# Performance work log

Measured on AMD Instinct MI355X. Metric: run time of the kernel, lower is better.

Reference implementation:

```python
import jax, jax.numpy as jnp
import numpy as np


def _gcn_conv(x, W, b, src, dst, n_nodes):
    """PyG-style GCNConv: XW, symmetric deg^-1/2 normalization over edges
    (with self-loops already included in src/dst), scatter-add to targets, + bias."""
    xw = x @ W  # [N, F_out]
    ones = jnp.ones(src.shape[0], dtype=xw.dtype)
    deg = jax.ops.segment_sum(ones, dst, num_segments=n_nodes)  # in-degree incl. self-loops
    dinv = jnp.where(deg > 0, jax.lax.rsqrt(jnp.maximum(deg, 1.0)), 0.0)
    norm = dinv[src] * dinv[dst]                        # [E]
    msgs = xw[src] * norm[:, None]                      # [E, F_out] gather + scale
    out = jax.ops.segment_sum(msgs, dst, num_segments=n_nodes)  # scatter-add
    return out + b


def setup_inputs() -> dict:
    key = jax.random.key(0)
    k1, k2, k3, k4 = jax.random.split(key, 4)
    N, E = 100000, 1600000
    IN, HID, OUT = 128, 64, 64
    x = jax.random.normal(k1, (N, IN), dtype=jnp.float32)
    edge_index = jax.random.randint(k2, (2, E), 0, N, dtype=jnp.int64)
    W1 = jax.random.normal(k3, (IN, HID), dtype=jnp.float32) * (1.0 / np.sqrt(IN))
    b1 = jnp.zeros((HID,), dtype=jnp.float32)
    W2 = jax.random.normal(k4, (HID, OUT), dtype=jnp.float32) * (1.0 / np.sqrt(HID))
    b2 = jnp.zeros((OUT,), dtype=jnp.float32)
    return {"x": x, "edge_index": edge_index, "W1": W1, "b1": b1, "W2": W2, "b2": b2}


def reference(x, edge_index, W1, b1, W2, b2):
    n_nodes = x.shape[0]
    # add self-loops (PyG GCNConv default add_self_loops=True)
    loops = jnp.arange(n_nodes, dtype=edge_index.dtype)
    src = jnp.concatenate([edge_index[0], loops])
    dst = jnp.concatenate([edge_index[1], loops])
    h = _gcn_conv(x, W1, b1, src, dst, n_nodes)
    h = jax.nn.relu(h)
    z = _gcn_conv(h, W2, b2, src, dst, n_nodes)
    return z
```

## Files before the change

kernel.cpp:

```cpp
#include <hip/hip_runtime.h>

#define IN_F 128
#define HID_F 64
#define BKT_SHIFT 9
#define BKT_SIZE 512
#define CHUNK 4096

typedef unsigned short ushort_t;
typedef __attribute__((ext_vector_type(8))) short bf16x8;
typedef __attribute__((ext_vector_type(8))) unsigned short u16x8;
typedef __attribute__((ext_vector_type(4))) float f32x4;

__device__ inline ushort_t f2bf(float f) {
    unsigned u = __float_as_uint(f);
    u += 0x7FFFu + ((u >> 16) & 1u);
    return (ushort_t)(u >> 16);
}
__device__ inline float bf2f(ushort_t u) {
    return __uint_as_float((unsigned)u << 16);
}


__global__ __launch_bounds__(256) void k_hist_pack(const int* __restrict__ dst,
        int* __restrict__ ghist, int E, int nbE,
        const float* __restrict__ W1, const float* __restrict__ W2,
        ushort_t* __restrict__ Bp1, ushort_t* __restrict__ Bp2) {
    int tid = threadIdx.x;
    if ((int)blockIdx.x >= nbE) {
        int id = ((int)blockIdx.x - nbE) * 256 + tid;
        int iw = (id < 8192) ? id : id - 8192;
        int j = iw & 7, lane = (iw >> 3) & 63, t = (iw >> 9) & 3, s = iw >> 11;
        int k = s * 32 + ((lane >> 4) << 3) + j;
        int n = t * 16 + (lane & 15);
        if (id < 8192)        Bp1[iw] = f2bf(W1[k * 64 + n]);
        else if (id < 12288)  Bp2[iw] = f2bf(W2[k * 64 + n]);
        return;
    }
    __shared__ int hist[256];
    hist[tid] = 0;
    __syncthreads();
    int e0 = blockIdx.x * CHUNK, e1 = min(e0 + CHUNK, E);
    for (int e = e0 + tid; e < e1; e += 256)
        atomicAdd(&hist[dst[e] >> BKT_SHIFT], 1);
    __syncthreads();
    ghist[blockIdx.x * 256 + tid] = hist[tid];
}

__global__ __launch_bounds__(256) void k_colscan(int* __restrict__ ghist,
        int* __restrict__ gcount, int nb) {
    __shared__ int s[256];
    int t = threadIdx.x;
    int b = blockIdx.x;
    int j0 = 2 * t, j1 = 2 * t + 1;
    int v0 = (j0 < nb) ? ghist[j0 * 256 + b] : 0;
    int v1 = (j1 < nb) ? ghist[j1 * 256 + b] : 0;
    int p = v0 + v1;
    s[t] = p;
    __syncthreads();
    for (int off = 1; off < 256; off <<= 1) {
        int v = (t >= off) ? s[t - off] : 0;
        __syncthreads();
        s[t] += v;
        __syncthreads();
    }
    int excl = s[t] - p;
    if (j0 < nb) ghist[j0 * 256 + b] = excl;
    if (j1 < nb) ghist[j1 * 256 + b] = excl + v0;
    if (t == 255) gcount[b] = s[255];
}

__global__ __launch_bounds__(256) void k_scatter(const int* __restrict__ src,
        const int* __restrict__ dst, const int* __restrict__ ghist,
        const int* __restrict__ gcount, unsigned* __restrict__ gbin, int E) {
    __shared__ int cur[256];
    __shared__ int s[256];
    int tid = threadIdx.x;
    int gc = gcount[tid];
    s[tid] = gc;
    __syncthreads();
    for (int off = 1; off < 256; off <<= 1) {
        int v = (tid >= off) ? s[tid - off] : 0;
        __syncthreads();
        s[tid] += v;
        __syncthreads();
    }
    cur[tid] = ghist[blockIdx.x * 256 + tid] + (s[tid] - gc);
    __syncthreads();
    int e0 = blockIdx.x * CHUNK, e1 = min(e0 + CHUNK, E);
    for (int e = e0 + tid; e < e1; e += 256) {
        int d = dst[e];
        int b = d >> BKT_SHIFT;
        int p = atomicAdd(&cur[b], 1);
        gbin[p] = ((unsigned)(d & (BKT_SIZE - 1)) << 23) | (unsigned)src[e];
    }
}

__global__ __launch_bounds__(256) void k_fill2(const unsigned* __restrict__ gbin,
        const int* __restrict__ gcount, int* __restrict__ rowptr,
        float* __restrict__ dinv, int* __restrict__ col, int N, int E) {
    __shared__ int cnt[BKT_SIZE];
    __shared__ int pos[BKT_SIZE];
    __shared__ int s[256];
    int tid = threadIdx.x;
    int b = blockIdx.x;
    int gc = gcount[tid];
    s[tid] = gc;
    __syncthreads();
    for (int off = 1; off < 256; off <<= 1) {
        int v = (tid >= off) ? s[tid - off] : 0;
        __syncthreads();
        s[tid] += v;
        __syncthreads();
    }
    int e0 = (b > 0) ? s[b - 1] : 0;
    int e1 = s[b];
    if (b == 0 && tid == 0) rowptr[N] = E;
    __syncthreads();
    cnt[tid] = 0; cnt[tid + 256] = 0;
    __syncthreads();
    for (int e = e0 + tid; e < e1; e += 256)
        atomicAdd(&cnt[gbin[e] >> 23], 1);
    __syncthreads();
    int c0 = cnt[2 * tid], c1 = cnt[2 * tid + 1];
    int p2 = c0 + c1;
    s[tid] = p2;
    __syncthreads();
    for (int off = 1; off < 256; off <<= 1) {
        int v = (tid >= off) ? s[tid - off] : 0;
        __syncthreads();
        s[tid] += v;
        __syncthreads();
    }
    int excl = s[tid] - p2;
    pos[2 * tid] = excl;
    pos[2 * tid + 1] = excl + c0;
    __syncthreads();
    int n0 = b << BKT_SHIFT;
    #pragma unroll
    for (int i = tid; i < BKT_SIZE; i += 256) {
        int n = n0 + i;
        if (n < N) {
            rowptr[n] = e0 + pos[i];
            dinv[n] = rsqrtf((float)cnt[i] + 1.0f);
        }
    }
    __syncthreads();
    for (int e = e0 + tid; e < e1; e += 256) {
        unsigned v = gbin[e];
        int p = atomicAdd(&pos[v >> 23], 1);
        col[e0 + p] = (int)(v & 0x7FFFFFu);
    }
}

template<int K, typename AT>
__global__ __launch_bounds__(256) void k_gemm_mfma(const AT* __restrict__ A,
        const ushort_t* __restrict__ Bp, const float* __restrict__ dinv,
        ushort_t* __restrict__ out, int N) {
    int wave = threadIdx.x >> 6, lane = threadIdx.x & 63;
    int m = lane & 15, q = lane >> 4;
    int row0 = blockIdx.x * 64 + wave * 16;
    int arow = row0 + m;
    int arowc = (arow < N) ? arow : (N - 1);
    f32x4 acc[4] = {};
    #pragma unroll
    for (int s = 0; s < K / 32; ++s) {
        bf16x8 af;
        if constexpr (sizeof(AT) == 4) {
            const float* ap = (const float*)A + (size_t)arowc * K + s * 32 + q * 8;
            float4 x0 = *(const float4*)ap;
            float4 x1 = *(const float4*)(ap + 4);
            af[0] = (short)f2bf(x0.x); af[1] = (short)f2bf(x0.y);
            af[2] = (short)f2bf(x0.z); af[3] = (short)f2bf(x0.w);
            af[4] = (short)f2bf(x1.x); af[5] = (short)f2bf(x1.y);
            af[6] = (short)f2bf(x1.z); af[7] = (short)f2bf(x1.w);
        } else {
            af = *(const bf16x8*)((const ushort_t*)A + (size_t)arowc * K + s * 32 + q * 8);
        }
        #pragma unroll
        for (int t = 0; t < 4; ++t) {
            bf16x8 bf = *(const bf16x8*)(Bp + (size_t)((s * 4 + t) * 64 + lane) * 8);
            acc[t] = __builtin_amdgcn_mfma_f32_16x16x32_bf16(af, bf, acc[t], 0, 0, 0);
        }
    }
    int orow0 = row0 + q * 4;
    float4 d4 = *(const float4*)(dinv + orow0);
    #pragma unroll
    for (int r = 0; r < 4; ++r) {
        int row = orow0 + r;
        if (row < N) {
            float dn = (r == 0) ? d4.x : (r == 1) ? d4.y : (r == 2) ? d4.z : d4.w;
            #pragma unroll
            for (int t = 0; t < 4; ++t)
                out[(size_t)row * 64 + t * 16 + m] = f2bf(acc[t][r] * dn);
        }
    }
}

__global__ __launch_bounds__(256) void k_agg_gemm(const ushort_t* __restrict__ xws,
        const int* __restrict__ rowptr, const int* __restrict__ col,
        const float* __restrict__ dinv, const float* __restrict__ bias,
        const ushort_t* __restrict__ Bp2, ushort_t* __restrict__ out2, int N) {
    __shared__ ushort_t hl[32][72];
    int tid = threadIdx.x;
    int nl = tid >> 3;
    int i = tid & 7;
    int n0 = blockIdx.x * 32;
    int n = n0 + nl;
    u16x8 hz = {};
    if (n < N) {
        int beg = rowptr[n], end = rowptr[n + 1];
        float dn = dinv[n];
        const ushort_t* base = xws + i * 8;
        u16x8 sv = *(const u16x8*)(base + (size_t)n * 64);
        float a[8];
        #pragma unroll
        for (int k = 0; k < 8; ++k) a[k] = bf2f(sv[k]);
        int e = beg;
        for (; e + 8 <= end; e += 8) {
            int c[8];
            #pragma unroll
            for (int j = 0; j < 8; ++j) c[j] = col[e + j];
            u16x8 v[8];
            #pragma unroll
            for (int j = 0; j < 8; ++j) v[j] = *(const u16x8*)(base + (size_t)c[j] * 64);
            #pragma unroll
            for (int j = 0; j < 8; ++j)
                #pragma unroll
                for (int k = 0; k < 8; ++k) a[k] += bf2f(v[j][k]);
        }
        if (e + 4 <= end) {
            int c[4];
            #pragma unroll
            for (int j = 0; j < 4; ++j) c[j] = col[e + j];
            u16x8 v[4];
            #pragma unroll
            for (int j = 0; j < 4; ++j) v[j] = *(const u16x8*)(base + (size_t)c[j] * 64);
            #pragma unroll
            for (int j = 0; j < 4; ++j)
                #pragma unroll
                for (int k = 0; k < 8; ++k) a[k] += bf2f(v[j][k]);
            e += 4;
        }
        for (; e < end; ++e) {
            u16x8 v = *(const u16x8*)(base + (size_t)col[e] * 64);
            #pragma unroll
            for (int k = 0; k < 8; ++k) a[k] += bf2f(v[k]);
        }
        float4 b0 = *(const float4*)(bias + i * 8);
        float4 b1 = *(const float4*)(bias + i * 8 + 4);
        float r[8];
        r[0] = dn * a[0] + b0.x; r[1] = dn * a[1] + b0.y;
        r[2] = dn * a[2] + b0.z; r[3] = dn * a[3] + b0.w;
        r[4] = dn * a[4] + b1.x; r[5] = dn * a[5] + b1.y;
        r[6] = dn * a[6] + b1.z; r[7] = dn * a[7] + b1.w;
        #pragma unroll
        for (int k = 0; k < 8; ++k) hz[k] = f2bf(fmaxf(r[k], 0.f));
    }
    *(u16x8*)&hl[nl][i * 8] = hz;
    __syncthreads();
    int w = tid >> 6, lane = tid & 63;
    int m = lane & 15, q = lane >> 4;
    int mt = w & 1;
    int nt0 = (w >> 1) << 1;
    f32x4 acc[2] = {};
    #pragma unroll
    for (int s = 0; s < 2; ++s) {
        bf16x8 af = *(const bf16x8*)&hl[mt * 16 + m][s * 32 + q * 8];
        #pragma unroll
        for (int tt = 0; tt < 2; ++tt) {
            bf16x8 bf = *(const bf16x8*)(Bp2 + (size_t)((s * 4 + nt0 + tt) * 64 + lane) * 8);
            acc[tt] = __builtin_amdgcn_mfma_f32_16x16x32_bf16(af, bf, acc[tt], 0, 0, 0);
        }
    }
    int orow0 = n0 + mt * 16 + q * 4;
    float4 d4 = *(const float4*)(dinv + orow0);
    #pragma unroll
    for (int r = 0; r < 4; ++r) {
        int row = orow0 + r;
        if (row < N) {
            float dn = (r == 0) ? d4.x : (r == 1) ? d4.y : (r == 2) ? d4.z : d4.w;
            #pragma unroll
            for (int tt = 0; tt < 2; ++tt)
                out2[(size_t)row * 64 + (nt0 + tt) * 16 + m] = f2bf(acc[tt][r] * dn);
        }
    }
}

__global__ __launch_bounds__(256) void k_aggregate(const ushort_t* __restrict__ xws,
        const int* __restrict__ rowptr, const int* __restrict__ col,
        const float* __restrict__ dinv, const float* __restrict__ bias,
        float* __restrict__ outf, int N) {
    int n = (blockIdx.x * 256 + threadIdx.x) >> 3;
    int i = threadIdx.x & 7;
    if (n >= N) return;
    int beg = rowptr[n], end = rowptr[n + 1];
    float dn = dinv[n];
    const ushort_t* base = xws + i * 8;
    u16x8 sv = *(const u16x8*)(base + (size_t)n * 64);
    float a[8];
    #pragma unroll
    for (int k = 0; k < 8; ++k) a[k] = bf2f(sv[k]);
    int e = beg;
    for (; e + 8 <= end; e += 8) {
        int c[8];
        #pragma unroll
        for (int j = 0; j < 8; ++j) c[j] = col[e + j];
        u16x8 v[8];
        #pragma unroll
        for (int j = 0; j < 8; ++j) v[j] = *(const u16x8*)(base + (size_t)c[j] * 64);
        #pragma unroll
        for (int j = 0; j < 8; ++j)
            #pragma unroll
            for (int k = 0; k < 8; ++k) a[k] += bf2f(v[j][k]);
    }
    if (e + 4 <= end) {
        int c[4];
        #pragma unroll
        for (int j = 0; j < 4; ++j) c[j] = col[e + j];
        u16x8 v[4];
        #pragma unroll
        for (int j = 0; j < 4; ++j) v[j] = *(const u16x8*)(base + (size_t)c[j] * 64);
        #pragma unroll
        for (int j = 0; j < 4; ++j)
            #pragma unroll
            for (int k = 0; k < 8; ++k) a[k] += bf2f(v[j][k]);
        e += 4;
    }
    for (; e < end; ++e) {
        u16x8 v = *(const u16x8*)(base + (size_t)col[e] * 64);
        #pragma unroll
        for (int k = 0; k < 8; ++k) a[k] += bf2f(v[k]);
    }
    float4 b0 = *(const float4*)(bias + i * 8);
    float4 b1 = *(const float4*)(bias + i * 8 + 4);
    float4 o0 = {dn * a[0] + b0.x, dn * a[1] + b0.y, dn * a[2] + b0.z, dn * a[3] + b0.w};
    float4 o1 = {dn * a[4] + b1.x, dn * a[5] + b1.y, dn * a[6] + b1.z, dn * a[7] + b1.w};
    *(float4*)(outf + (size_t)n * 64 + i * 8) = o0;
    *(float4*)(outf + (size_t)n * 64 + i * 8 + 4) = o1;
}


extern "C" void kernel_launch(void* const* d_in, const int* in_sizes, int n_in,
                              void* d_out, int out_size, void* d_ws, size_t ws_size,
                              hipStream_t stream) {
    const float* x  = (const float*)d_in[0];
    const int*   ei = (const int*)d_in[1];
    const float* W1 = (const float*)d_in[2];
    const float* b1 = (const float*)d_in[3];
    const float* W2 = (const float*)d_in[4];
    const float* b2 = (const float*)d_in[5];
    float* out = (float*)d_out;

    const int N = in_sizes[0] / IN_F;
    const int E = in_sizes[1] / 2;
    const int* src = ei;
    const int* dst = ei + E;

    char* ws = (char*)d_ws;
    const size_t MB = 1u << 20;
    int*      gcount  = (int*)     (ws + 12288);
    ushort_t* Bp1     = (ushort_t*)(ws + 16384);
    ushort_t* Bp2     = (ushort_t*)(ws + 49152);
    int*      rowptr  = (int*)     (ws + 1 * MB);
    float*    dinv    = (float*)   (ws + 2 * MB);
    unsigned* gbin    = (unsigned*)(ws + 3 * MB);
    int*      ghist   = (int*)     (ws + 10 * MB);
    int*      col     = (int*)     (ws + 11 * MB);
    ushort_t* xws     = (ushort_t*)(ws + 20 * MB);
    ushort_t* xws2    = (ushort_t*)(ws + 36 * MB);

    const int nbE = (E + CHUNK - 1) / CHUNK;
    const int nbB = (N + BKT_SIZE - 1) / BKT_SIZE;
    const int nbG = (N + 63) / 64;
    const int nbA = (N * 8 + 255) / 256;

    k_hist_pack<<<nbE + 48, 256, 0, stream>>>(dst, ghist, E, nbE, W1, W2, Bp1, Bp2);
    k_colscan<<<256, 256, 0, stream>>>(ghist, gcount, nbE);
    k_scatter<<<nbE, 256, 0, stream>>>(src, dst, ghist, gcount, gbin, E);
    k_fill2  <<<nbB, 256, 0, stream>>>(gbin, gcount, rowptr, dinv, col, N, E);

    k_gemm_mfma<IN_F, float><<<nbG, 256, 0, stream>>>(x, Bp1, dinv, xws, N);
    k_agg_gemm<<<nbA, 256, 0, stream>>>(xws, rowptr, col, dinv, b1, Bp2, xws2, N);
    k_aggregate<<<nbA, 256, 0, stream>>>(xws2, rowptr, col, dinv, b2, out, N);
}
```

Baseline: 229.5 us.

## Compute degrees with global atomics and overlap first GEMM with CSR build kernels

Degree counts are now accumulated per node with global atomics during the histogram pass, and the normalization is recomputed from them, so k_fill2 no longer needs a local counting pass over the binned edges. The first GEMM kernel is removed: its row blocks are split across the colscan, scatter and fill kernels as extra blocks, so the dense transform runs concurrently with the CSR construction. A memset of the degree array is added. The cost is 1.6M global atomics on deg, which may contend, in exchange for one fewer launch and better use of the GPU during the latency-bound sort stages.

```diff
diff --git a/kernel.cpp b/kernel.cpp
--- a/kernel.cpp
+++ b/kernel.cpp
@@ -20,9 +20,50 @@
     return __uint_as_float((unsigned)u << 16);
 }
 
+__device__ inline void gemm1_block(int gb, const float* __restrict__ A,
+        const ushort_t* __restrict__ Bp, const int* __restrict__ deg,
+        ushort_t* __restrict__ out, int N) {
+    int tid = threadIdx.x;
+    int wave = tid >> 6, lane = tid & 63;
+    int m = lane & 15, q = lane >> 4;
+    int row0 = gb * 64 + wave * 16;
+    int arow = row0 + m;
+    int arowc = (arow < N) ? arow : (N - 1);
+    f32x4 acc[4] = {};
+    #pragma unroll
+    for (int s = 0; s < 4; ++s) {
+        const float* ap = A + (size_t)arowc * 128 + s * 32 + q * 8;
+        float4 x0 = *(const float4*)ap;
+        float4 x1 = *(const float4*)(ap + 4);
+        bf16x8 af;
+        af[0] = (short)f2bf(x0.x); af[1] = (short)f2bf(x0.y);
+        af[2] = (short)f2bf(x0.z); af[3] = (short)f2bf(x0.w);
+        af[4] = (short)f2bf(x1.x); af[5] = (short)f2bf(x1.y);
+        af[6] = (short)f2bf(x1.z); af[7] = (short)f2bf(x1.w);
+        #pragma unroll
+        for (int t = 0; t < 4; ++t) {
+            bf16x8 bf = *(const bf16x8*)(Bp + (size_t)((s * 4 + t) * 64 + lane) * 8);
+            acc[t] = __builtin_amdgcn_mfma_f32_16x16x32_bf16(af, bf, acc[t], 0, 0, 0);
+        }
+    }
+    int orow0 = row0 + q * 4;
+    int4 dg = *(const int4*)(deg + orow0);
+    #pragma unroll
+    for (int r = 0; r < 4; ++r) {
+        int row = orow0 + r;
+        if (row < N) {
+            int dv = (r == 0) ? dg.x : (r == 1) ? dg.y : (r == 2) ? dg.z : dg.w;
+            float dn = rsqrtf((float)dv + 1.0f);
+            #pragma unroll
+            for (int t = 0; t < 4; ++t)
+                out[(size_t)row * 64 + t * 16 + m] = f2bf(acc[t][r] * dn);
+        }
+    }
+}
+
 
 __global__ __launch_bounds__(256) void k_hist_pack(const int* __restrict__ dst,
-        int* __restrict__ ghist, int E, int nbE,
+        int* __restrict__ ghist, int* __restrict__ deg, int E, int nbE,
         const float* __restrict__ W1, const float* __restrict__ W2,
         ushort_t* __restrict__ Bp1, ushort_t* __restrict__ Bp2) {
     int tid = threadIdx.x;
@@ -40,14 +81,23 @@
     hist[tid] = 0;
     __syncthreads();
     int e0 = blockIdx.x * CHUNK, e1 = min(e0 + CHUNK, E);
-    for (int e = e0 + tid; e < e1; e += 256)
-        atomicAdd(&hist[dst[e] >> BKT_SHIFT], 1);
+    for (int e = e0 + tid; e < e1; e += 256) {
+        int d = dst[e];
+        atomicAdd(&hist[d >> BKT_SHIFT], 1);
+        atomicAdd(&deg[d], 1);
+    }
     __syncthreads();
     ghist[blockIdx.x * 256 + tid] = hist[tid];
 }
 
 __global__ __launch_bounds__(256) void k_colscan(int* __restrict__ ghist,
-        int* __restrict__ gcount, int nb) {
+        int* __restrict__ gcount, int nb,
+        const float* __restrict__ x, const ushort_t* __restrict__ Bp1,
+        const int* __restrict__ deg, ushort_t* __restrict__ xws, int N, int gbase) {
+    if ((int)blockIdx.x >= 256) {
+        gemm1_block(gbase + (int)blockIdx.x - 256, x, Bp1, deg, xws, N);
+        return;
+    }
     __shared__ int s[256];
     int t = threadIdx.x;
     int b = blockIdx.x;
@@ -71,7 +121,13 @@
 
 __global__ __launch_bounds__(256) void k_scatter(const int* __restrict__ src,
         const int* __restrict__ dst, const int* __restrict__ ghist,
-        const int* __restrict__ gcount, unsigned* __restrict__ gbin, int E) {
+        const int* __restrict__ gcount, unsigned* __restrict__ gbin, int E, int nbE,
+        const float* __restrict__ x, const ushort_t* __restrict__ Bp1,
+        const int* __restrict__ deg, ushort_t* __restrict__ xws, int N, int gbase) {
+    if ((int)blockIdx.x >= nbE) {
+        gemm1_block(gbase + (int)blockIdx.x - nbE, x, Bp1, deg, xws, N);
+        return;
+    }
     __shared__ int cur[256];
     __shared__ int s[256];
     int tid = threadIdx.x;
@@ -96,8 +152,14 @@
 }
 
 __global__ __launch_bounds__(256) void k_fill2(const unsigned* __restrict__ gbin,
-        const int* __restrict__ gcount, int* __restrict__ rowptr,
-        float* __restrict__ dinv, int* __restrict__ col, int N, int E) {
+        const int* __restrict__ gcount, const int* __restrict__ deg,
+        int* __restrict__ rowptr, int* __restrict__ col, int N, int E, int nbB,
+        const float* __restrict__ x, const ushort_t* __restrict__ Bp1,
+        ushort_t* __restrict__ xws, int gbase) {
+    if ((int)blockIdx.x >= nbB) {
+        gemm1_block(gbase + (int)blockIdx.x - nbB, x, Bp1, deg, xws, N);
+        return;
+    }
     __shared__ int cnt[BKT_SIZE];
     __shared__ int pos[BKT_SIZE];
     __shared__ int s[256];
@@ -115,11 +177,12 @@
     int e0 = (b > 0) ? s[b - 1] : 0;
     int e1 = s[b];
     if (b == 0 && tid == 0) rowptr[N] = E;
-    __syncthreads();
-    cnt[tid] = 0; cnt[tid + 256] = 0;
-    __syncthreads();
-    for (int e = e0 + tid; e < e1; e += 256)
-        atomicAdd(&cnt[gbin[e] >> 23], 1);
+    int n0 = b << BKT_SHIFT;
+    {
+        int na = n0 + tid, nb2 = n0 + 256 + tid;
+        cnt[tid]       = (na  < N) ? deg[na]  : 0;
+        cnt[tid + 256] = (nb2 < N) ? deg[nb2] : 0;
+    }
     __syncthreads();
     int c0 = cnt[2 * tid], c1 = cnt[2 * tid + 1];
     int p2 = c0 + c1;
@@ -135,14 +198,10 @@
     pos[2 * tid] = excl;
     pos[2 * tid + 1] = excl + c0;
     __syncthreads();
-    int n0 = b << BKT_SHIFT;
     #pragma unroll
     for (int i = tid; i < BKT_SIZE; i += 256) {
         int n = n0 + i;
-        if (n < N) {
-            rowptr[n] = e0 + pos[i];
-            dinv[n] = rsqrtf((float)cnt[i] + 1.0f);
-        }
+        if (n < N) rowptr[n] = e0 + pos[i];
     }
     __syncthreads();
     for (int e = e0 + tid; e < e1; e += 256) {
@@ -152,53 +211,9 @@
     }
 }
 
-template<int K, typename AT>
-__global__ __launch_bounds__(256) void k_gemm_mfma(const AT* __restrict__ A,
-        const ushort_t* __restrict__ Bp, const float* __restrict__ dinv,
-        ushort_t* __restrict__ out, int N) {
-    int wave = threadIdx.x >> 6, lane = threadIdx.x & 63;
-    int m = lane & 15, q = lane >> 4;
-    int row0 = blockIdx.x * 64 + wave * 16;
-    int arow = row0 + m;
-    int arowc = (arow < N) ? arow : (N - 1);
-    f32x4 acc[4] = {};
-    #pragma unroll
-    for (int s = 0; s < K / 32; ++s) {
-        bf16x8 af;
-        if constexpr (sizeof(AT) == 4) {
-            const float* ap = (const float*)A + (size_t)arowc * K + s * 32 + q * 8;
-            float4 x0 = *(const float4*)ap;
-            float4 x1 = *(const float4*)(ap + 4);
-            af[0] = (short)f2bf(x0.x); af[1] = (short)f2bf(x0.y);
-            af[2] = (short)f2bf(x0.z); af[3] = (short)f2bf(x0.w);
-            af[4] = (short)f2bf(x1.x); af[5] = (short)f2bf(x1.y);
-            af[6] = (short)f2bf(x1.z); af[7] = (short)f2bf(x1.w);
-        } else {
-            af = *(const bf16x8*)((const ushort_t*)A + (size_t)arowc * K + s * 32 + q * 8);
-        }
-        #pragma unroll
-        for (int t = 0; t < 4; ++t) {
-            bf16x8 bf = *(const bf16x8*)(Bp + (size_t)((s * 4 + t) * 64 + lane) * 8);
-            acc[t] = __builtin_amdgcn_mfma_f32_16x16x32_bf16(af, bf, acc[t], 0, 0, 0);
-        }
-    }
-    int orow0 = row0 + q * 4;
-    float4 d4 = *(const float4*)(dinv + orow0);
-    #pragma unroll
-    for (int r = 0; r < 4; ++r) {
-        int row = orow0 + r;
-        if (row < N) {
-            float dn = (r == 0) ? d4.x : (r == 1) ? d4.y : (r == 2) ? d4.z : d4.w;
-            #pragma unroll
-            for (int t = 0; t < 4; ++t)
-                out[(size_t)row * 64 + t * 16 + m] = f2bf(acc[t][r] * dn);
-        }
-    }
-}
-
 __global__ __launch_bounds__(256) void k_agg_gemm(const ushort_t* __restrict__ xws,
         const int* __restrict__ rowptr, const int* __restrict__ col,
-        const float* __restrict__ dinv, const float* __restrict__ bias,
+        const int* __restrict__ deg, const float* __restrict__ bias,
         const ushort_t* __restrict__ Bp2, ushort_t* __restrict__ out2, int N) {
     __shared__ ushort_t hl[32][72];
     int tid = threadIdx.x;
@@ -209,7 +224,7 @@
     u16x8 hz = {};
     if (n < N) {
         int beg = rowptr[n], end = rowptr[n + 1];
-        float dn = dinv[n];
+        float dn = rsqrtf((float)deg[n] + 1.0f);
         const ushort_t* base = xws + i * 8;
         u16x8 sv = *(const u16x8*)(base + (size_t)n * 64);
         float a[8];
@@ -273,12 +288,13 @@
         }
     }
     int orow0 = n0 + mt * 16 + q * 4;
-    float4 d4 = *(const float4*)(dinv + orow0);
+    int4 dg = *(const int4*)(deg + orow0);
     #pragma unroll
     for (int r = 0; r < 4; ++r) {
         int row = orow0 + r;
         if (row < N) {
-            float dn = (r == 0) ? d4.x : (r == 1) ? d4.y : (r == 2) ? d4.z : d4.w;
+            int dv = (r == 0) ? dg.x : (r == 1) ? dg.y : (r == 2) ? dg.z : dg.w;
+            float dn = rsqrtf((float)dv + 1.0f);
             #pragma unroll
             for (int tt = 0; tt < 2; ++tt)
                 out2[(size_t)row * 64 + (nt0 + tt) * 16 + m] = f2bf(acc[tt][r] * dn);
@@ -288,13 +304,13 @@
 
 __global__ __launch_bounds__(256) void k_aggregate(const ushort_t* __restrict__ xws,
         const int* __restrict__ rowptr, const int* __restrict__ col,
-        const float* __restrict__ dinv, const float* __restrict__ bias,
+        const int* __restrict__ deg, const float* __restrict__ bias,
         float* __restrict__ outf, int N) {
     int n = (blockIdx.x * 256 + threadIdx.x) >> 3;
     int i = threadIdx.x & 7;
     if (n >= N) return;
     int beg = rowptr[n], end = rowptr[n + 1];
-    float dn = dinv[n];
+    float dn = rsqrtf((float)deg[n] + 1.0f);
     const ushort_t* base = xws + i * 8;
     u16x8 sv = *(const u16x8*)(base + (size_t)n * 64);
     float a[8];
@@ -362,7 +378,7 @@
     ushort_t* Bp1     = (ushort_t*)(ws + 16384);
     ushort_t* Bp2     = (ushort_t*)(ws + 49152);
     int*      rowptr  = (int*)     (ws + 1 * MB);
-    float*    dinv    = (float*)   (ws + 2 * MB);
+    int*      deg     = (int*)     (ws + 2 * MB);
     unsigned* gbin    = (unsigned*)(ws + 3 * MB);
     int*      ghist   = (int*)     (ws + 10 * MB);
     int*      col     = (int*)     (ws + 11 * MB);
@@ -374,12 +390,19 @@
     const int nbG = (N + 63) / 64;
     const int nbA = (N * 8 + 255) / 256;
 
-    k_hist_pack<<<nbE + 48, 256, 0, stream>>>(dst, ghist, E, nbE, W1, W2, Bp1, Bp2);
-    k_colscan<<<256, 256, 0, stream>>>(ghist, gcount, nbE);
-    k_scatter<<<nbE, 256, 0, stream>>>(src, dst, ghist, gcount, gbin, E);
-    k_fill2  <<<nbB, 256, 0, stream>>>(gbin, gcount, rowptr, dinv, col, N, E);
-
-    k_gemm_mfma<IN_F, float><<<nbG, 256, 0, stream>>>(x, Bp1, dinv, xws, N);
-    k_agg_gemm<<<nbA, 256, 0, stream>>>(xws, rowptr, col, dinv, b1, Bp2, xws2, N);
-    k_aggregate<<<nbA, 256, 0, stream>>>(xws2, rowptr, col, dinv, b2, out, N);
-}
+    const int g0 = (nbG < 300) ? nbG : 300;
+    const int g1 = (nbG - g0 < 700) ? (nbG - g0) : 700;
+    const int g2 = nbG - g0 - g1;
+
+    hipMemsetAsync(deg, 0, (size_t)N * sizeof(int), stream);
+    k_hist_pack<<<nbE + 48, 256, 0, stream>>>(dst, ghist, deg, E, nbE, W1, W2, Bp1, Bp2);
+    k_colscan<<<256 + g0, 256, 0, stream>>>(ghist, gcount, nbE,
+                                            x, Bp1, deg, xws, N, 0);
+    k_scatter<<<nbE + g1, 256, 0, stream>>>(src, dst, ghist, gcount, gbin, E, nbE,
+                                            x, Bp1, deg, xws, N, g0);
+    k_fill2  <<<nbB + g2, 256, 0, stream>>>(gbin, gcount, deg, rowptr, col, N, E, nbB,
+                                            x, Bp1, xws, g0 + g1);
+
+    k_agg_gemm<<<nbA, 256, 0, stream>>>(xws, rowptr, col, deg, b1, Bp2, xws2, N);
+    k_aggregate<<<nbA, 256, 0, stream>>>(xws2, rowptr, col, deg, b2, out, N);
+}
```

Result: slower. 277.0 us (+20.7%).
